# Performance work log

Hardware: AMD Instinct MI355X
Metric: run time of the kernel (lower is better)

## Reference

```python
import jax, jax.numpy as jnp
import numpy as np


def setup_inputs() -> dict:
    key = jax.random.key(0)
    k1, k2, k3, k4 = jax.random.split(key, 4)
    L, B, D, H = 512, 128, 512, 1024
    x = jax.random.normal(k1, (L, B, D), dtype=jnp.float32)
    Wx = jax.random.normal(k2, (H, D), dtype=jnp.float32) * (1.0 / np.sqrt(D))
    bx = jax.random.normal(k3, (H,), dtype=jnp.float32) * 0.01
    Wh = jax.random.normal(k4, (H, H), dtype=jnp.float32) * (1.0 / np.sqrt(H))
    return {"x": x, "Wx": Wx, "bx": bx, "Wh": Wh}


def reference(x, Wx, bx, Wh):
    # x: [L, B, D]; Wx: [H, D]; bx: [H]; Wh: [H, H]
    # h_t = tanh(x_t @ Wx^T + bx + h_{t-1} @ Wh^T), h_{-1} = 0
    L, B, D = x.shape
    H = Wx.shape[0]
    # Precompute the input projection for all timesteps in one big GEMM.
    xproj = jnp.einsum('lbd,hd->lbh', x, Wx) + bx  # [L, B, H]

    def step(h, xp_t):
        h_new = jnp.tanh(xp_t + h @ Wh.T)  # [B, H]
        return h_new, h_new

    h0 = jnp.zeros((B, H), dtype=x.dtype)
    _, hs = jax.lax.scan(step, h0, xproj)
    return hs  # [L, B, H]
```

## Files before the change

kernel.cpp:

```cpp
#include <hip/hip_runtime.h>
#include <math.h>


#define L_SEQ 512
#define B_SZ  128
#define H_SZ  1024
#define BH    (B_SZ * H_SZ)

typedef __bf16 bf16x8 __attribute__((ext_vector_type(8)));
typedef float  f32x4  __attribute__((ext_vector_type(4)));
typedef unsigned int uint;
typedef uint u32x4 __attribute__((ext_vector_type(4)));
typedef uint u32x2 __attribute__((ext_vector_type(2)));
typedef unsigned short ushort;

union V8 { bf16x8 b; ushort u[8]; };

__device__ __forceinline__ ushort f2bf(float f) {
  uint u = __float_as_uint(f);
  u += 0x7FFFu + ((u >> 16) & 1u);
  return (ushort)(u >> 16);
}
__device__ __forceinline__ float bf2f(ushort s) {
  return __uint_as_float(((uint)s) << 16);
}

__device__ __forceinline__ float fast_tanh(float x) {
  float e;
  asm("v_exp_f32 %0, %1" : "=v"(e) : "v"(x * 2.885390081777927f));
  float r;
  asm("v_rcp_f32 %0, %1" : "=v"(r) : "v"(e + 1.0f));
  return 1.0f - 2.0f * r;
}

__device__ __forceinline__ void ldg16_sc(u32x4& d, const uint* p) {
  asm volatile("global_load_dwordx4 %0, %1, off sc0 sc1"
               : "=v"(d) : "v"(p) : "memory");
}
__device__ __forceinline__ void stg8_sc(uint* p, u32x2 v) {
  asm volatile("global_store_dwordx2 %0, %1, off sc0 sc1"
               :: "v"(p), "v"(v) : "memory");
}

#define WS_WHH 0
#define WS_WHL 1048576
#define WS_WXH 2097152
#define WS_WXL 2621440

__global__ void split_kernel(const float* __restrict__ Wh,
                             const float* __restrict__ Wx,
                             ushort* __restrict__ ws) {
  const int total = 1048576 + 524288;
  for (int i = blockIdx.x * blockDim.x + threadIdx.x; i < total;
       i += gridDim.x * blockDim.x) {
    const float* src; ushort *dh, *dl; int j;
    if (i < 1048576) { src = Wh; dh = ws + WS_WHH; dl = ws + WS_WHL; j = i; }
    else             { src = Wx; dh = ws + WS_WXH; dl = ws + WS_WXL; j = i - 1048576; }
    float v = src[j];
    ushort h = f2bf(v);
    dh[j] = h;
    dl[j] = f2bf(v - bf2f(h));
  }
}

__global__ __launch_bounds__(256) void xproj_kernel(
    const float* __restrict__ x,
    const ushort* __restrict__ wxh,
    const ushort* __restrict__ wxl,
    const float* __restrict__ bx,
    float* __restrict__ out)
{
  const int bid = blockIdx.x;
  const int bn = bid & 15;
  const int bm = bid >> 4;
  const int tid = threadIdx.x;
  const int w = tid >> 6, l = tid & 63;
  const int wm = w & 1, wn = w >> 1;
  const int lr = l & 15, lk = (l >> 4) * 8;
  const int mbase = bm * 128 + wm * 64;
  const int nbase = bn * 64 + wn * 32;

  f32x4 acc[4][2] = {};

  for (int k0 = 0; k0 < 512; k0 += 32) {
    bf16x8 ah[4], al[4], bh[2], bl[2];
#pragma unroll
    for (int i = 0; i < 4; ++i) {
      const float* ap = x + (size_t)(mbase + i * 16 + lr) * 512 + k0 + lk;
      float4 v0 = *reinterpret_cast<const float4*>(ap);
      float4 v1 = *reinterpret_cast<const float4*>(ap + 4);
      float vv[8] = {v0.x, v0.y, v0.z, v0.w, v1.x, v1.y, v1.z, v1.w};
      V8 hh, ll;
#pragma unroll
      for (int e = 0; e < 8; ++e) {
        ushort hb = f2bf(vv[e]);
        hh.u[e] = hb;
        ll.u[e] = f2bf(vv[e] - bf2f(hb));
      }
      ah[i] = hh.b; al[i] = ll.b;
    }
#pragma unroll
    for (int j = 0; j < 2; ++j) {
      size_t boff = (size_t)(nbase + j * 16 + lr) * 512 + k0 + lk;
      bh[j] = *reinterpret_cast<const bf16x8*>(wxh + boff);
      bl[j] = *reinterpret_cast<const bf16x8*>(wxl + boff);
    }
#pragma unroll
    for (int i = 0; i < 4; ++i)
#pragma unroll
      for (int j = 0; j < 2; ++j) {
        acc[i][j] = __builtin_amdgcn_mfma_f32_16x16x32_bf16(ah[i], bh[j], acc[i][j], 0, 0, 0);
        acc[i][j] = __builtin_amdgcn_mfma_f32_16x16x32_bf16(ah[i], bl[j], acc[i][j], 0, 0, 0);
        acc[i][j] = __builtin_amdgcn_mfma_f32_16x16x32_bf16(al[i], bh[j], acc[i][j], 0, 0, 0);
      }
  }

#pragma unroll
  for (int j = 0; j < 2; ++j) {
    int n = nbase + j * 16 + lr;
    float bxv = bx[n];
#pragma unroll
    for (int i = 0; i < 4; ++i)
#pragma unroll
      for (int r = 0; r < 4; ++r) {
        int m = mbase + i * 16 + (l >> 4) * 4 + r;
        out[(size_t)m * 1024 + n] = acc[i][j][r] + bxv;
      }
  }
}

__global__ __launch_bounds__(512, 2) void rnn_persistent(
    const ushort* __restrict__ whh,
    const ushort* __restrict__ whl,
    uint* __restrict__ hbt,
    float* __restrict__ out)
{
  __shared__ uint smraw[16384];
  ushort* lds_hi = (ushort*)smraw;
  ushort* lds_lo = lds_hi + 16384;
  float*  part   = (float*)smraw;

  const int wg = blockIdx.x;
  const int g  = wg & 7;
  const int c  = wg >> 3;
  const int tid = threadIdx.x;
  const int w = tid >> 6, l = tid & 63;
  const int lr = l & 15, lq = l >> 4;

  bf16x8 vBh[4][4], vBl[4][4];
#pragma unroll
  for (int ct = 0; ct < 4; ++ct)
#pragma unroll
    for (int ck = 0; ck < 4; ++ck) {
      size_t a = (size_t)(c * 64 + ct * 16 + lr) * 1024 + w * 128 + ck * 32 + lq * 8;
      vBh[ct][ck] = *reinterpret_cast<const bf16x8*>(whh + a);
      vBl[ct][ck] = *reinterpret_cast<const bf16x8*>(whl + a);
    }

  const int e0 = tid * 2;
  const int row0 = e0 >> 6, cw0 = e0 & 63;
  const int row1 = (e0 + 1) >> 6, cw1 = (e0 + 1) & 63;
  const size_t oidx0 = (size_t)(g * 16 + row0) * 1024 + c * 64 + cw0;
  const size_t oidx1 = (size_t)(g * 16 + row1) * 1024 + c * 64 + cw1;

  const uint* pollbase[2];
  pollbase[0] = hbt + (((size_t)g * 16384 + w * 2048 + l * 2) << 1);
  pollbase[1] = hbt + (((size_t)BH + g * 16384 + w * 2048 + l * 2) << 1);

  {
    float h0 = fast_tanh(out[oidx0]);
    float h1 = fast_tanh(out[oidx1]);
    out[oidx0] = h0;
    out[oidx1] = h1;
    ushort hh0 = f2bf(h0), hh1 = f2bf(h1);
    u32x2 v0, v1;
    v0[0] = ((uint)hh0 << 16) | (uint)f2bf(h0 - bf2f(hh0)); v0[1] = 1u;
    v1[0] = ((uint)hh1 << 16) | (uint)f2bf(h1 - bf2f(hh1)); v1[1] = 1u;
    stg8_sc(hbt + (oidx0 << 1), v0);
    stg8_sc(hbt + (oidx1 << 1), v1);
  }

  for (int t = 1; t < L_SEQ; ++t) {
    float* xpt = out + (size_t)t * BH;
    const float xpv0 = xpt[oidx0];
    const float xpv1 = xpt[oidx1];

    const uint* pb = pollbase[(t - 1) & 1];
    const uint tg = (uint)t;
    u32x4 d[16];
    for (uint spin = 0; spin < (1u << 20); ++spin) {
      #pragma unroll
      for (int i = 0; i < 16; ++i) ldg16_sc(d[i], pb + (i << 8));
      asm volatile("s_waitcnt vmcnt(0)" ::: "memory");
      __builtin_amdgcn_sched_barrier(0);
      bool ok = true;
      #pragma unroll
      for (int i = 0; i < 16; ++i) ok = ok && (d[i][1] == tg) && (d[i][3] == tg);
      if (__all((int)ok)) break;
      __builtin_amdgcn_s_sleep(1);
    }
    __builtin_amdgcn_sched_barrier(0);

    #pragma unroll
    for (int i = 0; i < 16; ++i) {
      const int e = w * 2048 + i * 128 + l * 2;
      const int row = e >> 10, k = e & 1023;
      const int u = ((k >> 3) << 4) + row;
      const int pos = k & 7;
      uint hip = (d[i][0] >> 16) | (d[i][2] & 0xFFFF0000u);
      uint lop = (d[i][0] & 0xFFFFu) | (d[i][2] << 16);
      *reinterpret_cast<uint*>(lds_hi + u * 8 + pos) = hip;
      *reinterpret_cast<uint*>(lds_lo + u * 8 + pos) = lop;
    }
    __syncthreads();

    bf16x8 vAh[4], vAl[4];
    #pragma unroll
    for (int ck = 0; ck < 4; ++ck) {
      const int u = ((w * 16 + ck * 4 + lq) << 4) + lr;
      vAh[ck] = *reinterpret_cast<const bf16x8*>(lds_hi + u * 8);
      vAl[ck] = *reinterpret_cast<const bf16x8*>(lds_lo + u * 8);
    }
    __syncthreads();

    f32x4 acc[4] = {};
    #pragma unroll
    for (int ct = 0; ct < 4; ++ct)
      #pragma unroll
      for (int ck = 0; ck < 4; ++ck) {
        acc[ct] = __builtin_amdgcn_mfma_f32_16x16x32_bf16(vAh[ck], vBh[ct][ck], acc[ct], 0, 0, 0);
        acc[ct] = __builtin_amdgcn_mfma_f32_16x16x32_bf16(vAh[ck], vBl[ct][ck], acc[ct], 0, 0, 0);
        acc[ct] = __builtin_amdgcn_mfma_f32_16x16x32_bf16(vAl[ck], vBh[ct][ck], acc[ct], 0, 0, 0);
      }

    #pragma unroll
    for (int ct = 0; ct < 4; ++ct)
      #pragma unroll
      for (int r = 0; r < 4; ++r)
        part[w * 1088 + (ct * 16 + lr) * 17 + lq * 4 + r] = acc[ct][r];
    __syncthreads();

    float s0 = 0.f, s1 = 0.f;
    #pragma unroll
    for (int q = 0; q < 8; ++q) {
      s0 += part[q * 1088 + cw0 * 17 + row0];
      s1 += part[q * 1088 + cw1 * 17 + row1];
    }
    float h0 = fast_tanh(s0 + xpv0);
    float h1 = fast_tanh(s1 + xpv1);
    ushort hh0 = f2bf(h0), hh1 = f2bf(h1);
    u32x2 v0, v1;
    v0[0] = ((uint)hh0 << 16) | (uint)f2bf(h0 - bf2f(hh0)); v0[1] = tg + 1u;
    v1[0] = ((uint)hh1 << 16) | (uint)f2bf(h1 - bf2f(hh1)); v1[1] = tg + 1u;
    uint* planew = hbt + ((size_t)(t & 1) * BH << 1);
    stg8_sc(planew + (oidx0 << 1), v0);
    stg8_sc(planew + (oidx1 << 1), v1);
    xpt[oidx0] = h0;
    xpt[oidx1] = h1;
  }
}

extern "C" void kernel_launch(void* const* d_in, const int* in_sizes, int n_in,
                              void* d_out, int out_size, void* d_ws, size_t ws_size,
                              hipStream_t stream) {
  const float* x  = (const float*)d_in[0];
  const float* Wx = (const float*)d_in[1];
  const float* bx = (const float*)d_in[2];
  const float* Wh = (const float*)d_in[3];
  float* out = (float*)d_out;
  ushort* ws = (ushort*)d_ws;

  ushort* whh = ws + WS_WHH;
  ushort* whl = ws + WS_WHL;
  ushort* wxh = ws + WS_WXH;
  ushort* wxl = ws + WS_WXL;
  uint*   hbt = (uint*)(ws + WS_WXH);

  split_kernel<<<dim3(2048), dim3(256), 0, stream>>>(Wh, Wx, ws);
  xproj_kernel<<<dim3(8192), dim3(256), 0, stream>>>(x, wxh, wxl, bx, out);
  rnn_persistent<<<dim3(128), dim3(512), 0, stream>>>(whh, whl, hbt, out);
}
```

Before: 4.150 ms.

## Pack tag into low bits of h, double block count, load A directly from global

The persistent RNN now runs 256 workgroups, each owning 32 output columns instead of 64. The step tag is packed into the two low bits of the bf16 lo word, so each exchanged hidden value is a single 32-bit store instead of an 8-byte value+tag pair. Each wave loads its own MFMA A-fragments straight from global memory and re-polls only the chunks that are not ready, which removes the LDS transpose and two barriers per step. The partial-sum buffer is double-buffered so one barrier per step suffices. The trade-off is a little precision loss in the lo term from masking two bits, and more workgroups taking part in the cross-workgroup synchronisation.

```diff
diff --git a/kernel.cpp b/kernel.cpp
--- a/kernel.cpp
+++ b/kernel.cpp
@@ -11,10 +11,9 @@
 typedef float  f32x4  __attribute__((ext_vector_type(4)));
 typedef unsigned int uint;
 typedef uint u32x4 __attribute__((ext_vector_type(4)));
-typedef uint u32x2 __attribute__((ext_vector_type(2)));
 typedef unsigned short ushort;
 
-union V8 { bf16x8 b; ushort u[8]; };
+union V8 { bf16x8 b; ushort u[8]; uint w[4]; };
 
 __device__ __forceinline__ ushort f2bf(float f) {
   uint u = __float_as_uint(f);
@@ -37,8 +36,8 @@
   asm volatile("global_load_dwordx4 %0, %1, off sc0 sc1"
                : "=v"(d) : "v"(p) : "memory");
 }
-__device__ __forceinline__ void stg8_sc(uint* p, u32x2 v) {
-  asm volatile("global_store_dwordx2 %0, %1, off sc0 sc1"
+__device__ __forceinline__ void stg4_sc(uint* p, uint v) {
+  asm volatile("global_store_dword %0, %1, off sc0 sc1"
                :: "v"(p), "v"(v) : "memory");
 }
 
@@ -46,13 +45,16 @@
 #define WS_WHL 1048576
 #define WS_WXH 2097152
 #define WS_WXL 2621440
+#define WS_HBT 3145728
 
 __global__ void split_kernel(const float* __restrict__ Wh,
                              const float* __restrict__ Wx,
-                             ushort* __restrict__ ws) {
+                             ushort* __restrict__ ws,
+                             uint* __restrict__ hbt) {
+  const int gid = blockIdx.x * blockDim.x + threadIdx.x;
+  if (gid < 2 * BH) hbt[gid] = 0u;
   const int total = 1048576 + 524288;
-  for (int i = blockIdx.x * blockDim.x + threadIdx.x; i < total;
-       i += gridDim.x * blockDim.x) {
+  for (int i = gid; i < total; i += gridDim.x * blockDim.x) {
     const float* src; ushort *dh, *dl; int j;
     if (i < 1048576) { src = Wh; dh = ws + WS_WHH; dl = ws + WS_WHL; j = i; }
     else             { src = Wx; dh = ws + WS_WXH; dl = ws + WS_WXL; j = i - 1048576; }
@@ -135,11 +137,7 @@
     uint* __restrict__ hbt,
     float* __restrict__ out)
 {
-  __shared__ uint smraw[16384];
-  ushort* lds_hi = (ushort*)smraw;
-  ushort* lds_lo = lds_hi + 16384;
-  float*  part   = (float*)smraw;
-
+  __shared__ float part[2][8][544];
   const int wg = blockIdx.x;
   const int g  = wg & 7;
   const int c  = wg >> 3;
@@ -147,116 +145,110 @@
   const int w = tid >> 6, l = tid & 63;
   const int lr = l & 15, lq = l >> 4;
 
-  bf16x8 vBh[4][4], vBl[4][4];
-#pragma unroll
-  for (int ct = 0; ct < 4; ++ct)
-#pragma unroll
-    for (int ck = 0; ck < 4; ++ck) {
-      size_t a = (size_t)(c * 64 + ct * 16 + lr) * 1024 + w * 128 + ck * 32 + lq * 8;
+  bf16x8 vBh[2][4], vBl[2][4];
+#pragma unroll
+  for (int ct = 0; ct < 2; ++ct)
+#pragma unroll
+    for (int ck = 0; ck < 4; ++ck) {
+      size_t a = (size_t)(c * 32 + ct * 16 + lr) * 1024 + w * 128 + ck * 32 + lq * 8;
       vBh[ct][ck] = *reinterpret_cast<const bf16x8*>(whh + a);
       vBl[ct][ck] = *reinterpret_cast<const bf16x8*>(whl + a);
     }
 
-  const int e0 = tid * 2;
-  const int row0 = e0 >> 6, cw0 = e0 & 63;
-  const int row1 = (e0 + 1) >> 6, cw1 = (e0 + 1) & 63;
-  const size_t oidx0 = (size_t)(g * 16 + row0) * 1024 + c * 64 + cw0;
-  const size_t oidx1 = (size_t)(g * 16 + row1) * 1024 + c * 64 + cw1;
-
-  const uint* pollbase[2];
-  pollbase[0] = hbt + (((size_t)g * 16384 + w * 2048 + l * 2) << 1);
-  pollbase[1] = hbt + (((size_t)BH + g * 16384 + w * 2048 + l * 2) << 1);
+  const size_t aoff = (size_t)(g * 16 + lr) * 1024 + w * 128 + lq * 8;
+
+  const int erow = tid & 15, ecol = tid >> 4;
+  const size_t oidx = (size_t)(g * 16 + erow) * 1024 + c * 32 + ecol;
 
   {
-    float h0 = fast_tanh(out[oidx0]);
-    float h1 = fast_tanh(out[oidx1]);
-    out[oidx0] = h0;
-    out[oidx1] = h1;
-    ushort hh0 = f2bf(h0), hh1 = f2bf(h1);
-    u32x2 v0, v1;
-    v0[0] = ((uint)hh0 << 16) | (uint)f2bf(h0 - bf2f(hh0)); v0[1] = 1u;
-    v1[0] = ((uint)hh1 << 16) | (uint)f2bf(h1 - bf2f(hh1)); v1[1] = 1u;
-    stg8_sc(hbt + (oidx0 << 1), v0);
-    stg8_sc(hbt + (oidx1 << 1), v1);
+    float h = fast_tanh(out[oidx]);
+    out[oidx] = h;
+    ushort hh = f2bf(h);
+    ushort ll = f2bf(h - bf2f(hh));
+    stg4_sc(hbt + oidx, ((uint)hh << 16) | ((uint)ll & 0xFFFCu) | 1u);
   }
 
   for (int t = 1; t < L_SEQ; ++t) {
-    float* xpt = out + (size_t)t * BH;
-    const float xpv0 = xpt[oidx0];
-    const float xpv1 = xpt[oidx1];
-
-    const uint* pb = pollbase[(t - 1) & 1];
-    const uint tg = (uint)t;
-    u32x4 d[16];
+    const uint tagv  = (uint)((t - 1) % 3) + 1u;
+    const uint mytag = (uint)(t % 3) + 1u;
+    const uint* pb = hbt + (size_t)((t - 1) & 1) * BH + aoff;
+    const float xpv = out[(size_t)t * BH + oidx];
+
+    u32x4 d[8];
+#pragma unroll
+    for (int ck = 0; ck < 4; ++ck) {
+      ldg16_sc(d[2 * ck],     pb + ck * 32);
+      ldg16_sc(d[2 * ck + 1], pb + ck * 32 + 4);
+    }
+    asm volatile("s_waitcnt vmcnt(0)" ::: "memory");
     for (uint spin = 0; spin < (1u << 20); ++spin) {
-      #pragma unroll
-      for (int i = 0; i < 16; ++i) ldg16_sc(d[i], pb + (i << 8));
+      bool ok[4]; bool allok = true;
+#pragma unroll
+      for (int ck = 0; ck < 4; ++ck) {
+        uint xo = (d[2*ck][0] ^ tagv) | (d[2*ck][1] ^ tagv) |
+                  (d[2*ck][2] ^ tagv) | (d[2*ck][3] ^ tagv) |
+                  (d[2*ck+1][0] ^ tagv) | (d[2*ck+1][1] ^ tagv) |
+                  (d[2*ck+1][2] ^ tagv) | (d[2*ck+1][3] ^ tagv);
+        ok[ck] = ((xo & 3u) == 0u);
+        allok = allok && ok[ck];
+      }
+      if (__all((int)allok)) break;
+      __builtin_amdgcn_s_sleep(2);
+#pragma unroll
+      for (int ck = 0; ck < 4; ++ck) {
+        if (!ok[ck]) {
+          ldg16_sc(d[2 * ck],     pb + ck * 32);
+          ldg16_sc(d[2 * ck + 1], pb + ck * 32 + 4);
+        }
+      }
       asm volatile("s_waitcnt vmcnt(0)" ::: "memory");
-      __builtin_amdgcn_sched_barrier(0);
-      bool ok = true;
-      #pragma unroll
-      for (int i = 0; i < 16; ++i) ok = ok && (d[i][1] == tg) && (d[i][3] == tg);
-      if (__all((int)ok)) break;
-      __builtin_amdgcn_s_sleep(1);
     }
     __builtin_amdgcn_sched_barrier(0);
 
-    #pragma unroll
-    for (int i = 0; i < 16; ++i) {
-      const int e = w * 2048 + i * 128 + l * 2;
-      const int row = e >> 10, k = e & 1023;
-      const int u = ((k >> 3) << 4) + row;
-      const int pos = k & 7;
-      uint hip = (d[i][0] >> 16) | (d[i][2] & 0xFFFF0000u);
-      uint lop = (d[i][0] & 0xFFFFu) | (d[i][2] << 16);
-      *reinterpret_cast<uint*>(lds_hi + u * 8 + pos) = hip;
-      *reinterpret_cast<uint*>(lds_lo + u * 8 + pos) = lop;
+    bf16x8 vAh[4], vAl[4];
+#pragma unroll
+    for (int ck = 0; ck < 4; ++ck) {
+      V8 hh, ll;
+#pragma unroll
+      for (int i = 0; i < 2; ++i) {
+        const u32x4 p = d[2 * ck + i];
+        hh.w[2*i]   = (p[0] >> 16) | (p[1] & 0xFFFF0000u);
+        hh.w[2*i+1] = (p[2] >> 16) | (p[3] & 0xFFFF0000u);
+        ll.w[2*i]   = (p[0] & 0xFFFCu) | ((p[1] & 0xFFFCu) << 16);
+        ll.w[2*i+1] = (p[2] & 0xFFFCu) | ((p[3] & 0xFFFCu) << 16);
+      }
+      vAh[ck] = hh.b; vAl[ck] = ll.b;
+    }
+
+    f32x4 acc0 = {0.f, 0.f, 0.f, 0.f};
+    f32x4 acc1 = {0.f, 0.f, 0.f, 0.f};
+#pragma unroll
+    for (int ck = 0; ck < 4; ++ck) {
+      acc0 = __builtin_amdgcn_mfma_f32_16x16x32_bf16(vAh[ck], vBh[0][ck], acc0, 0, 0, 0);
+      acc1 = __builtin_amdgcn_mfma_f32_16x16x32_bf16(vAh[ck], vBh[1][ck], acc1, 0, 0, 0);
+      acc0 = __builtin_amdgcn_mfma_f32_16x16x32_bf16(vAh[ck], vBl[0][ck], acc0, 0, 0, 0);
+      acc1 = __builtin_amdgcn_mfma_f32_16x16x32_bf16(vAh[ck], vBl[1][ck], acc1, 0, 0, 0);
+      acc0 = __builtin_amdgcn_mfma_f32_16x16x32_bf16(vAl[ck], vBh[0][ck], acc0, 0, 0, 0);
+      acc1 = __builtin_amdgcn_mfma_f32_16x16x32_bf16(vAl[ck], vBh[1][ck], acc1, 0, 0, 0);
+    }
+
+    float* pp = &part[t & 1][w][0];
+#pragma unroll
+    for (int r = 0; r < 4; ++r) {
+      pp[(lr) * 17      + lq * 4 + r] = acc0[r];
+      pp[(16 + lr) * 17 + lq * 4 + r] = acc1[r];
     }
     __syncthreads();
 
-    bf16x8 vAh[4], vAl[4];
-    #pragma unroll
-    for (int ck = 0; ck < 4; ++ck) {
-      const int u = ((w * 16 + ck * 4 + lq) << 4) + lr;
-      vAh[ck] = *reinterpret_cast<const bf16x8*>(lds_hi + u * 8);
-      vAl[ck] = *reinterpret_cast<const bf16x8*>(lds_lo + u * 8);
-    }
-    __syncthreads();
-
-    f32x4 acc[4] = {};
-    #pragma unroll
-    for (int ct = 0; ct < 4; ++ct)
-      #pragma unroll
-      for (int ck = 0; ck < 4; ++ck) {
-        acc[ct] = __builtin_amdgcn_mfma_f32_16x16x32_bf16(vAh[ck], vBh[ct][ck], acc[ct], 0, 0, 0);
-        acc[ct] = __builtin_amdgcn_mfma_f32_16x16x32_bf16(vAh[ck], vBl[ct][ck], acc[ct], 0, 0, 0);
-        acc[ct] = __builtin_amdgcn_mfma_f32_16x16x32_bf16(vAl[ck], vBh[ct][ck], acc[ct], 0, 0, 0);
-      }
-
-    #pragma unroll
-    for (int ct = 0; ct < 4; ++ct)
-      #pragma unroll
-      for (int r = 0; r < 4; ++r)
-        part[w * 1088 + (ct * 16 + lr) * 17 + lq * 4 + r] = acc[ct][r];
-    __syncthreads();
-
-    float s0 = 0.f, s1 = 0.f;
-    #pragma unroll
-    for (int q = 0; q < 8; ++q) {
-      s0 += part[q * 1088 + cw0 * 17 + row0];
-      s1 += part[q * 1088 + cw1 * 17 + row1];
-    }
-    float h0 = fast_tanh(s0 + xpv0);
-    float h1 = fast_tanh(s1 + xpv1);
-    ushort hh0 = f2bf(h0), hh1 = f2bf(h1);
-    u32x2 v0, v1;
-    v0[0] = ((uint)hh0 << 16) | (uint)f2bf(h0 - bf2f(hh0)); v0[1] = tg + 1u;
-    v1[0] = ((uint)hh1 << 16) | (uint)f2bf(h1 - bf2f(hh1)); v1[1] = tg + 1u;
-    uint* planew = hbt + ((size_t)(t & 1) * BH << 1);
-    stg8_sc(planew + (oidx0 << 1), v0);
-    stg8_sc(planew + (oidx1 << 1), v1);
-    xpt[oidx0] = h0;
-    xpt[oidx1] = h1;
+    float s = 0.f;
+#pragma unroll
+    for (int q = 0; q < 8; ++q) s += part[t & 1][q][ecol * 17 + erow];
+    float h = fast_tanh(s + xpv);
+    out[(size_t)t * BH + oidx] = h;
+    ushort hh = f2bf(h);
+    ushort ll = f2bf(h - bf2f(hh));
+    stg4_sc(hbt + (size_t)(t & 1) * BH + oidx,
+            ((uint)hh << 16) | ((uint)ll & 0xFFFCu) | mytag);
   }
 }
 
@@ -274,9 +266,9 @@
   ushort* whl = ws + WS_WHL;
   ushort* wxh = ws + WS_WXH;
   ushort* wxl = ws + WS_WXL;
-  uint*   hbt = (uint*)(ws + WS_WXH);
-
-  split_kernel<<<dim3(2048), dim3(256), 0, stream>>>(Wh, Wx, ws);
+  uint*   hbt = (uint*)(ws + WS_HBT);
+
+  split_kernel<<<dim3(2048), dim3(256), 0, stream>>>(Wh, Wx, ws, hbt);
   xproj_kernel<<<dim3(8192), dim3(256), 0, stream>>>(x, wxh, wxl, bx, out);
-  rnn_persistent<<<dim3(128), dim3(512), 0, stream>>>(whh, whl, hbt, out);
-}
+  rnn_persistent<<<dim3(256), dim3(512), 0, stream>>>(whh, whl, hbt, out);
+}
```

After: 5.869 ms. 41.4% more time.
